# Kernel optimization log

Hardware: AMD Instinct MI355X
Metric: run time of the kernel (lower is better)

The kernel has to match this reference:

```python
import jax, jax.numpy as jnp
import numpy as np

B, N, PLANE, H, W = 2, 6, 64, 48, 48
HIDP = 64
PS = 3
RATES = 3


def conv2d(x, w, b, pad, dil=1):
    # x: [BN, Cin, H, W], w: [Cout, Cin, kh, kw]
    out = jax.lax.conv_general_dilated(
        x, w, window_strides=(1, 1),
        padding=[(pad, pad), (pad, pad)],
        rhs_dilation=(dil, dil),
        dimension_numbers=('NCHW', 'OIHW', 'NCHW'))
    return out + b[None, :, None, None]


def avgpool3(x):
    bn, c, h, w = x.shape
    return x.reshape(bn, c, h // PS, PS, w // PS, PS).mean(axis=(3, 5))


def setup_inputs() -> dict:
    key = jax.random.key(0)
    ks = jax.random.split(key, 20)
    s = 0.05
    hid_pa = PLANE * 3  # 192, hidden width of MultiFieldConv2d
    d = {
        'x': jax.random.normal(ks[0], (B, N, PLANE, H, W), jnp.float32),
        # patch_aggr: 3 dilated convs (rates 1..3), k=3, plane -> plane*3
        'pa_w1': jax.random.normal(ks[1], (hid_pa, PLANE, 3, 3)) * s,
        'pa_b1': jnp.zeros((hid_pa,)),
        'pa_w2': jax.random.normal(ks[2], (hid_pa, PLANE, 3, 3)) * s,
        'pa_b2': jnp.zeros((hid_pa,)),
        'pa_w3': jax.random.normal(ks[3], (hid_pa, PLANE, 3, 3)) * s,
        'pa_b3': jnp.zeros((hid_pa,)),
        # convert: 1x1 (hid_pa*rates -> 3*hidp), relu, 1x1 (3*hidp -> 3*hidp)
        'pa_cw1': jax.random.normal(ks[4], (3 * HIDP, hid_pa * RATES, 1, 1)) * s,
        'pa_cb1': jnp.zeros((3 * HIDP,)),
        'pa_cw2': jax.random.normal(ks[5], (3 * HIDP, 3 * HIDP, 1, 1)) * s,
        'pa_cb2': jnp.zeros((3 * HIDP,)),
        # to_kv conv: k=3 pad=1, hidp -> hidp
        'kv_w': jax.random.normal(ks[6], (HIDP, HIDP, 3, 3)) * s,
        'kv_b': jnp.zeros((HIDP,)),
        # to_out: 1x1 hidp->plane, relu, 1x1 plane->plane, relu
        'out_w1': jax.random.normal(ks[7], (PLANE, HIDP, 1, 1)) * s,
        'out_b1': jnp.zeros((PLANE,)),
        'out_w2': jax.random.normal(ks[8], (PLANE, PLANE, 1, 1)) * s,
        'out_b2': jnp.zeros((PLANE,)),
        'scales': jnp.ones((N,)),
    }
    return d


def reference(x, pa_w1, pa_b1, pa_w2, pa_b2, pa_w3, pa_b3,
              pa_cw1, pa_cb1, pa_cw2, pa_cb2,
              kv_w, kv_b, out_w1, out_b1, out_w2, out_b2, scales):
    b, n, c, h, w = x.shape
    scale = HIDP ** (-0.5)
    xf = x.reshape(b * n, c, h, w)

    # MultiFieldConv2d: dilated convs (same spatial size for odd k), concat, 1x1 convert
    u = jnp.concatenate([
        conv2d(xf, pa_w1, pa_b1, pad=1, dil=1),
        conv2d(xf, pa_w2, pa_b2, pad=2, dil=2),
        conv2d(xf, pa_w3, pa_b3, pad=3, dil=3),
    ], axis=1)
    qkv = conv2d(jax.nn.relu(conv2d(u, pa_cw1, pa_cb1, 0)), pa_cw2, pa_cb2, 0)
    qkv = jax.nn.relu(qkv)  # F.relu(patch_aggr(x))
    xq, xk, xv = jnp.split(qkv, 3, axis=1)  # each [BN, hidp, H, W]

    def to_kv(t):
        return avgpool3(jax.nn.relu(conv2d(t, kv_w, kv_b, pad=PS // 2)))

    k_ = to_kv(xk)                       # [BN, hidp, H/3, W/3]
    v_ = to_kv(xv) * (1.0 / PS ** 2)

    hw_kv = k_.shape[2] * k_.shape[3]
    Qs = xq.reshape(b, n, HIDP, h * w).transpose(0, 1, 3, 2)   # b n g d
    Ks = k_.reshape(b, n, HIDP, hw_kv).transpose(0, 1, 3, 2)   # b m k d
    Vs = v_.reshape(b, n, HIDP, hw_kv).transpose(0, 1, 3, 2)

    # Leave-one-out sigmoid attention: sum_{j != i} sigmoid(q_i k_j^T * scale) @ v_j
    # Computed as full sum minus the self (j == i) term (exact same math).
    A_all = jax.nn.sigmoid(jnp.einsum('bngd,bmkd->bngmk', Qs, Ks) * scale)
    out_all = jnp.einsum('bngmk,bmkd->bngd', A_all, Vs)
    A_self = jax.nn.sigmoid(jnp.einsum('bngd,bnkd->bngk', Qs, Ks) * scale)
    out_self = jnp.einsum('bngk,bnkd->bngd', A_self, Vs)
    attn_out = out_all - out_self                               # [b, n, HW, hidp]

    res = attn_out.transpose(0, 1, 3, 2).reshape(b, n, HIDP, h, w)
    xv5 = xv.reshape(b, n, HIDP, h, w)
    res = jax.nn.relu(res + scales[None, :, None, None, None] * xv5)

    rf = res.reshape(b * n, HIDP, h, w)
    o = jax.nn.relu(conv2d(jax.nn.relu(conv2d(rf, out_w1, out_b1, 0)), out_w2, out_b2, 0))
    return o.reshape(b, n, c, h, w)
```

## Files before the change

kernel.cpp:

```cpp
#include <hip/hip_runtime.h>
#include <hip/hip_bf16.h>
#include <math.h>

#define BB 2
#define NVIEW 6
#define BN 12
#define CIN 64
#define HH 48
#define WW 48
#define PP (HH*WW)
#define OC 192
#define HPA 192
#define HIDP 64
#define KHW 16
#define PK 256
#define PADW 54
#define PADA (PADW*PADW)
#define NTOT (BN*PP)
#define K1 1728
#define KVPW 50
#define KVPA (KVPW*KVPW)

typedef __attribute__((ext_vector_type(8))) short bf16x8;
typedef __attribute__((ext_vector_type(4))) float f32x4;

#define OFF_WEFFB 0
#define SZ_WEFFB_FL (OC*K1/2)
#define OFF_BEFF (OFF_WEFFB + SZ_WEFFB_FL)
#define SZ_BEFF 256
#define OFF_CW2B (OFF_BEFF + SZ_BEFF)
#define SZ_CW2B_FL (OC*OC/2)
#define OFF_WKVB (OFF_CW2B + SZ_CW2B_FL)
#define SZ_WKVB_FL (64*576/2)
#define OFF_PADXT (OFF_WKVB + SZ_WKVB_FL)
#define SZ_PADXT_FL (BN*PADA*64/2)
#define OFF_QB16 (OFF_PADXT + SZ_PADXT_FL)
#define SZ_QB16_FL (BN*PP*64/2)
#define OFF_KB16 (OFF_QB16 + SZ_QB16_FL)
#define SZ_KB16_FL (BN*PK*64/2)
#define OFF_VB16T (OFF_KB16 + SZ_KB16_FL)
#define SZ_VB16T_FL (BN*64*PK/2)
#define OFF_KVPAD (OFF_VB16T + SZ_VB16T_FL)
#define SZ_KVPAD_FL (BN*2*KVPA*64/2)
#define OFF_CONVB (OFF_KVPAD + SZ_KVPAD_FL)
#define SZ_CONVB_FL (BN*2*PP*64/2)
#define OFF_W1SW (OFF_CONVB + SZ_CONVB_FL)
#define SZ_WSW_FL 2048
#define OFF_W2SW (OFF_W1SW + SZ_WSW_FL)
#define OFF_ATTNP (OFF_W2SW + SZ_WSW_FL)
#define SZ_ATTNP (BN*PP*HIDP)
#define OFF_XVB16 (OFF_ATTNP + 2*SZ_ATTNP)
#define SZ_XVB16_FL (BN*PP*64/2)

__device__ __forceinline__ void load_lds16(const void* g, void* l) {
    __builtin_amdgcn_global_load_lds(
        (const __attribute__((address_space(1))) unsigned int*)g,
        (__attribute__((address_space(3))) unsigned int*)l, 16, 0, 0);
}

__device__ __forceinline__ unsigned short f2bu(float f) {
    __hip_bfloat16 h = __float2bfloat16(f);
    return *(unsigned short*)&h;
}

__device__ __forceinline__ float bu2f(unsigned short h) {
    unsigned int u = ((unsigned int)h) << 16;
    return *(float*)&u;
}

__global__ void k_fold(const float* __restrict__ cw1, const float* __restrict__ cb1,
                       const float* __restrict__ w1, const float* __restrict__ b1,
                       const float* __restrict__ w2, const float* __restrict__ b2,
                       const float* __restrict__ w3, const float* __restrict__ b3,
                       __hip_bfloat16* __restrict__ weffb, float* __restrict__ beff) {
    int r = blockIdx.x / OC;
    int o = blockIdx.x % OC;
    int t = threadIdx.x;
    int ic = t / 9, tap = t % 9;
    const float* w = (r==0) ? w1 : (r==1) ? w2 : w3;
    float acc = 0.f;
    for (int c = 0; c < HPA; ++c)
        acc += cw1[o*(HPA*3) + r*HPA + c] * w[c*(CIN*9) + t];
    weffb[(size_t)o*K1 + r*576 + tap*64 + ic] = __float2bfloat16(acc);
    if (r == 0 && t == 0) {
        float bacc = cb1[o];
        for (int rr = 0; rr < 3; ++rr) {
            const float* bb = (rr==0)?b1:(rr==1)?b2:b3;
            for (int c = 0; c < HPA; ++c)
                bacc += cw1[o*(HPA*3) + rr*HPA + c] * bb[c];
        }
        beff[o] = bacc;
    }
}

__global__ void k_wkvb(const float* __restrict__ kvw, __hip_bfloat16* __restrict__ wkvb) {
    int idx = blockIdx.x*256 + threadIdx.x;
    if (idx >= 64*576) return;
    int oc = idx / 576, rest = idx % 576;
    int tap = rest / 64, ic = rest % 64;
    wkvb[idx] = __float2bfloat16(kvw[(oc*64 + ic)*9 + tap]);
}

__global__ void k_wcvt(const float* __restrict__ cw2, __hip_bfloat16* __restrict__ cw2b) {
    int idx = blockIdx.x*256 + threadIdx.x;
    if (idx < OC*OC) cw2b[idx] = __float2bfloat16(cw2[idx]);
}

__global__ void k_wout(const float* __restrict__ w1, const float* __restrict__ w2,
                       __hip_bfloat16* __restrict__ w1sw, __hip_bfloat16* __restrict__ w2sw) {
    int idx = blockIdx.x*256 + threadIdx.x;
    if (idx >= 2*4096) return;
    const float* w = (idx < 4096) ? w1 : w2;
    __hip_bfloat16* dst = (idx < 4096) ? w1sw : w2sw;
    int i = idx & 4095;
    int oc = i >> 6, s = (i >> 3) & 7, e = i & 7;
    int k = ((s ^ (oc & 7)) << 3) + e;
    dst[i] = __float2bfloat16(w[oc*64 + k]);
}

__global__ void k_padxT(const float* __restrict__ x, __hip_bfloat16* __restrict__ padxT) {
    int idx = blockIdx.x*256 + threadIdx.x;
    if (idx >= BN*PADA) return;
    int spos = idx % PADA; int bn = idx / PADA;
    int sy = spos / PADW, sx = spos % PADW;
    __hip_bfloat16* dst = padxT + (size_t)idx*64;
    if (sy >= 3 && sy < 51 && sx >= 3 && sx < 51) {
        const float* src = x + (size_t)bn*CIN*PP + (sy-3)*WW + (sx-3);
        #pragma unroll 8
        for (int ic = 0; ic < 64; ++ic) dst[ic] = __float2bfloat16(src[ic*PP]);
    } else {
        #pragma unroll 8
        for (int ic = 0; ic < 64; ++ic) dst[ic] = __float2bfloat16(0.f);
    }
}

__global__ void k_zero(__hip_bfloat16* __restrict__ kvpad) {
    size_t idx = ((size_t)blockIdx.x*256 + threadIdx.x)*8;
    bf16x8 z = (bf16x8){0,0,0,0,0,0,0,0};
    *(bf16x8*)(kvpad + idx) = z;
}

__global__ __launch_bounds__(256) void k_gemm1(const __hip_bfloat16* __restrict__ wA,
        const __hip_bfloat16* __restrict__ pxT, const float* __restrict__ beff,
        __hip_bfloat16* __restrict__ hidbt) {
    __shared__ __align__(16) char smem[24576];
    int tid = threadIdx.x;
    int wid = tid >> 6, lane = tid & 63;
    int tileN = blockIdx.x * 128, tileM = blockIdx.y * 64;
    int sgr = ((lane&7) ^ (lane>>3)) * 8;

    size_t gbase[6];
    #pragma unroll
    for (int s2 = 0; s2 < 6; ++s2) {
        int seg = wid*6 + s2;
        if (seg < 8) {
            int row = seg*8 + (lane>>3);
            gbase[s2] = (size_t)(tileM + row)*K1 + sgr;
        } else {
            int n = tileN + (seg-8)*8 + (lane>>3);
            int bn = n / PP, p = n % PP;
            int py = p / WW, px = p % WW;
            gbase[s2] = ((size_t)bn*PADA + (py+3)*PADW + (px+3))*64 + sgr;
        }
    }
    int wr = wid >> 1, wc = wid & 1;
    int l7 = lane & 7, lh = lane >> 4;
    int arowb[2], browb[4];
    #pragma unroll
    for (int m = 0; m < 2; ++m)
        arowb[m] = (wr*32 + m*16 + (lane&15))*128;
    #pragma unroll
    for (int nf = 0; nf < 4; ++nf)
        browb[nf] = 8192 + (wc*64 + nf*16 + (lane&15))*128;

    f32x4 acc[2][4];
    #pragma unroll
    for (int m = 0; m < 2; ++m)
        #pragma unroll
        for (int nf = 0; nf < 4; ++nf) acc[m][nf] = (f32x4){0.f,0.f,0.f,0.f};

    for (int kt = 0; kt < 27; ++kt) {
        int r_ = kt / 9, tap = kt - r_*9;
        int dy = tap/3 - 1, dx = tap%3 - 1;
        int doff = (r_+1)*(dy*PADW + dx);
        __syncthreads();
        #pragma unroll
        for (int s2 = 0; s2 < 6; ++s2) {
            int seg = wid*6 + s2;
            const __hip_bfloat16* g = (seg < 8) ? wA + gbase[s2] + kt*64
                                                : pxT + gbase[s2] + (size_t)doff*64;
            load_lds16(g, smem + seg*1024);
        }
        __syncthreads();
        bf16x8 a[2][2], b[4][2];
        #pragma unroll
        for (int kk = 0; kk < 2; ++kk) {
            int gof = ((kk*4 + lh) ^ l7) << 4;
            #pragma unroll
            for (int m = 0; m < 2; ++m)
                a[m][kk] = *(const bf16x8*)(smem + arowb[m] + gof);
            #pragma unroll
            for (int nf = 0; nf < 4; ++nf)
                b[nf][kk] = *(const bf16x8*)(smem + browb[nf] + gof);
        }
        #pragma unroll
        for (int kk = 0; kk < 2; ++kk)
            #pragma unroll
            for (int m = 0; m < 2; ++m)
                #pragma unroll
                for (int nf = 0; nf < 4; ++nf)
                    acc[m][nf] = __builtin_amdgcn_mfma_f32_16x16x32_bf16(
                        a[m][kk], b[nf][kk], acc[m][nf], 0, 0, 0);
    }
    #pragma unroll
    for (int m = 0; m < 2; ++m) {
        int rbase = tileM + wr*32 + m*16 + (lane>>4)*4;
        float4 bz = *(const float4*)&beff[rbase];
        #pragma unroll
        for (int nf = 0; nf < 4; ++nf) {
            int col = tileN + wc*64 + nf*16 + (lane&15);
            union { ushort4 u; __hip_bfloat16 h[4]; } cv;
            cv.h[0] = __float2bfloat16(fmaxf(acc[m][nf][0] + bz.x, 0.f));
            cv.h[1] = __float2bfloat16(fmaxf(acc[m][nf][1] + bz.y, 0.f));
            cv.h[2] = __float2bfloat16(fmaxf(acc[m][nf][2] + bz.z, 0.f));
            cv.h[3] = __float2bfloat16(fmaxf(acc[m][nf][3] + bz.w, 0.f));
            *(ushort4*)&hidbt[(size_t)col*OC + rbase] = cv.u;
        }
    }
}

__global__ __launch_bounds__(256) void k_gemm2(const __hip_bfloat16* __restrict__ wA,
        const __hip_bfloat16* __restrict__ Bt, const float* __restrict__ cb2,
        __hip_bfloat16* __restrict__ xvb16, __hip_bfloat16* __restrict__ qb16,
        __hip_bfloat16* __restrict__ kvpad) {
    __shared__ __align__(16) char smem[24576];
    int tid = threadIdx.x;
    int wid = tid >> 6, lane = tid & 63;
    int tileN = blockIdx.x * 128, tileM = blockIdx.y * 64;
    int sgr = ((lane&7) ^ (lane>>3)) * 8;
    size_t gbase[6]; const __hip_bfloat16* gsrc[6];
    #pragma unroll
    for (int s2 = 0; s2 < 6; ++s2) {
        int seg = wid*6 + s2;
        if (seg < 8) {
            int row = seg*8 + (lane>>3);
            gbase[s2] = (size_t)(tileM + row)*OC + sgr;
            gsrc[s2] = wA;
        } else {
            int n = tileN + (seg-8)*8 + (lane>>3);
            gbase[s2] = (size_t)n*OC + sgr;
            gsrc[s2] = Bt;
        }
    }
    int wr = wid >> 1, wc = wid & 1;
    int l7 = lane & 7, lh = lane >> 4;
    int arowb[2], browb[4];
    #pragma unroll
    for (int m = 0; m < 2; ++m)
        arowb[m] = (wr*32 + m*16 + (lane&15))*128;
    #pragma unroll
    for (int nf = 0; nf < 4; ++nf)
        browb[nf] = 8192 + (wc*64 + nf*16 + (lane&15))*128;
    f32x4 acc[2][4];
    #pragma unroll
    for (int m = 0; m < 2; ++m)
        #pragma unroll
        for (int nf = 0; nf < 4; ++nf) acc[m][nf] = (f32x4){0.f,0.f,0.f,0.f};

    for (int kt = 0; kt < 3; ++kt) {
        __syncthreads();
        #pragma unroll
        for (int s2 = 0; s2 < 6; ++s2)
            load_lds16(gsrc[s2] + gbase[s2] + kt*64, smem + (wid*6+s2)*1024);
        __syncthreads();
        bf16x8 a[2][2], b[4][2];
        #pragma unroll
        for (int kk = 0; kk < 2; ++kk) {
            int gof = ((kk*4 + lh) ^ l7) << 4;
            #pragma unroll
            for (int m = 0; m < 2; ++m)
                a[m][kk] = *(const bf16x8*)(smem + arowb[m] + gof);
            #pragma unroll
            for (int nf = 0; nf < 4; ++nf)
                b[nf][kk] = *(const bf16x8*)(smem + browb[nf] + gof);
        }
        #pragma unroll
        for (int kk = 0; kk < 2; ++kk)
            #pragma unroll
            for (int m = 0; m < 2; ++m)
                #pragma unroll
                for (int nf = 0; nf < 4; ++nf)
                    acc[m][nf] = __builtin_amdgcn_mfma_f32_16x16x32_bf16(
                        a[m][kk], b[nf][kk], acc[m][nf], 0, 0, 0);
    }
    #pragma unroll
    for (int m = 0; m < 2; ++m) {
        int rbase = tileM + wr*32 + m*16 + (lane>>4)*4;
        float4 cz = *(const float4*)&cb2[rbase];
        #pragma unroll
        for (int nf = 0; nf < 4; ++nf) {
            int col = tileN + wc*64 + nf*16 + (lane&15);
            int bn = col / PP, p = col % PP;
            float v0 = fmaxf(acc[m][nf][0] + cz.x, 0.f);
            float v1 = fmaxf(acc[m][nf][1] + cz.y, 0.f);
            float v2 = fmaxf(acc[m][nf][2] + cz.z, 0.f);
            float v3 = fmaxf(acc[m][nf][3] + cz.w, 0.f);
            ushort4 bv;
            bv.x = f2bu(v0); bv.y = f2bu(v1); bv.z = f2bu(v2); bv.w = f2bu(v3);
            if (tileM == 0) {
                *(ushort4*)&qb16[(size_t)col*64 + rbase] = bv;
            } else {
                int kv = (tileM == 128) ? 1 : 0;
                int py = p / WW, px = p % WW;
                int d = rbase - tileM;
                *(ushort4*)&kvpad[((size_t)(bn*2+kv)*KVPA + (py+1)*KVPW + px+1)*64 + d] = bv;
                if (kv == 1)
                    *(ushort4*)&xvb16[(size_t)col*64 + d] = bv;
            }
        }
    }
}

__global__ __launch_bounds__(256) void k_kvgemm(const __hip_bfloat16* __restrict__ wA,
        const __hip_bfloat16* __restrict__ kvpad, const float* __restrict__ kvb,
        __hip_bfloat16* __restrict__ convb) {
    __shared__ __align__(16) char smem[24576];
    int tid = threadIdx.x;
    int wid = tid >> 6, lane = tid & 63;
    int tileN = blockIdx.x * 128;
    int bn2 = tileN / PP, p0 = tileN % PP;
    int sgr = ((lane&7) ^ (lane>>3)) * 8;

    size_t gbase[6];
    #pragma unroll
    for (int s2 = 0; s2 < 6; ++s2) {
        int seg = wid*6 + s2;
        if (seg < 8) {
            int row = seg*8 + (lane>>3);
            gbase[s2] = (size_t)row*576 + sgr;
        } else {
            int p = p0 + (seg-8)*8 + (lane>>3);
            int py = p / WW, px = p % WW;
            gbase[s2] = ((size_t)bn2*KVPA + (py+1)*KVPW + px+1)*64 + sgr;
        }
    }
    int wr = wid >> 1, wc = wid & 1;
    int l7 = lane & 7, lh = lane >> 4;
    int arowb[2], browb[4];
    #pragma unroll
    for (int m = 0; m < 2; ++m)
        arowb[m] = (wr*32 + m*16 + (lane&15))*128;
    #pragma unroll
    for (int nf = 0; nf < 4; ++nf)
        browb[nf] = 8192 + (wc*64 + nf*16 + (lane&15))*128;

    f32x4 acc[2][4];
    #pragma unroll
    for (int m = 0; m < 2; ++m)
        #pragma unroll
        for (int nf = 0; nf < 4; ++nf) acc[m][nf] = (f32x4){0.f,0.f,0.f,0.f};

    for (int kt = 0; kt < 9; ++kt) {
        int dy = kt/3 - 1, dx = kt%3 - 1;
        int doff = dy*KVPW + dx;
        __syncthreads();
        #pragma unroll
        for (int s2 = 0; s2 < 6; ++s2) {
            int seg = wid*6 + s2;
            const __hip_bfloat16* g = (seg < 8) ? wA + gbase[s2] + kt*64
                                                : kvpad + gbase[s2] + (size_t)doff*64;
            load_lds16(g, smem + seg*1024);
        }
        __syncthreads();
        bf16x8 a[2][2], b[4][2];
        #pragma unroll
        for (int kk = 0; kk < 2; ++kk) {
            int gof = ((kk*4 + lh) ^ l7) << 4;
            #pragma unroll
            for (int m = 0; m < 2; ++m)
                a[m][kk] = *(const bf16x8*)(smem + arowb[m] + gof);
            #pragma unroll
            for (int nf = 0; nf < 4; ++nf)
                b[nf][kk] = *(const bf16x8*)(smem + browb[nf] + gof);
        }
        #pragma unroll
        for (int kk = 0; kk < 2; ++kk)
            #pragma unroll
            for (int m = 0; m < 2; ++m)
                #pragma unroll
                for (int nf = 0; nf < 4; ++nf)
                    acc[m][nf] = __builtin_amdgcn_mfma_f32_16x16x32_bf16(
                        a[m][kk], b[nf][kk], acc[m][nf], 0, 0, 0);
    }
    #pragma unroll
    for (int m = 0; m < 2; ++m) {
        int rbase = wr*32 + m*16 + (lane>>4)*4;
        float4 bz = *(const float4*)&kvb[rbase];
        #pragma unroll
        for (int nf = 0; nf < 4; ++nf) {
            int col = p0 + wc*64 + nf*16 + (lane&15);
            ushort4 cv;
            cv.x = f2bu(fmaxf(acc[m][nf][0] + bz.x, 0.f));
            cv.y = f2bu(fmaxf(acc[m][nf][1] + bz.y, 0.f));
            cv.z = f2bu(fmaxf(acc[m][nf][2] + bz.z, 0.f));
            cv.w = f2bu(fmaxf(acc[m][nf][3] + bz.w, 0.f));
            *(ushort4*)&convb[((size_t)bn2*PP + col)*64 + rbase] = cv;
        }
    }
}

__global__ __launch_bounds__(256) void k_pool(const __hip_bfloat16* __restrict__ convb,
        __hip_bfloat16* __restrict__ kbufb, __hip_bfloat16* __restrict__ vbufT) {
    int idx = blockIdx.x*256 + threadIdx.x;
    int dg = idx % 8; idx /= 8;
    int pp = idx % PK; idx /= PK;
    int bn2 = idx;
    int kv = bn2 & 1, bn = bn2 >> 1;
    int qy = pp / KHW, qx = pp % KHW;
    float s[8] = {0,0,0,0,0,0,0,0};
    const __hip_bfloat16* base = convb + (size_t)bn2*PP*64 + dg*8;
    #pragma unroll
    for (int sy = 0; sy < 3; ++sy)
        #pragma unroll
        for (int sx = 0; sx < 3; ++sx) {
            union { bf16x8 v; unsigned short h[8]; } c;
            c.v = *(const bf16x8*)(base + ((size_t)(qy*3+sy)*WW + qx*3+sx)*64);
            #pragma unroll
            for (int j = 0; j < 8; ++j) s[j] += bu2f(c.h[j]);
        }
    if (kv == 0) {
        union { ushort4 u[2]; unsigned short h[8]; } cv;
        #pragma unroll
        for (int j = 0; j < 8; ++j) cv.h[j] = f2bu(s[j] * (1.f/9.f));
        ushort4* dst = (ushort4*)(kbufb + ((size_t)bn*PK + pp)*64 + dg*8);
        dst[0] = cv.u[0]; dst[1] = cv.u[1];
    } else {
        #pragma unroll
        for (int j = 0; j < 8; ++j)
            vbufT[((size_t)bn*64 + dg*8 + j)*PK + pp] = __float2bfloat16(s[j]*(1.f/81.f));
    }
}

__global__ __launch_bounds__(256) void k_attn3(const __hip_bfloat16* __restrict__ qb16,
        const __hip_bfloat16* __restrict__ kbufb, const __hip_bfloat16* __restrict__ vbufT,
        float* __restrict__ attnp) {
    __shared__ __align__(16) char smem[32768];
    char* Qs = smem;
    char* Ks = smem + 8192;
    char* Vs = smem + 16384;
    char* Ps = smem + 24576;
    int tid = threadIdx.x;
    int wid = tid >> 6, lane = tid & 63;
    int bid = blockIdx.x;
    int ks = bid & 1; bid >>= 1;
    int qt = bid % 36; int bn = bid / 36;
    int b = bn / NVIEW, n = bn % NVIEW;
    int p0 = qt*64;

    {
        const char* gq = (const char*)(qb16 + ((size_t)bn*PP + p0)*64);
        #pragma unroll
        for (int i = 0; i < 2; ++i) {
            int s = wid*2 + i;
            int lin = s*1024 + lane*16;
            int r = lin >> 7, c = (lin >> 4) & 7;
            int gof = (r<<7) + ((c ^ (r&7)) << 4);
            load_lds16(gq + gof, Qs + s*1024);
        }
    }
    int arow = wid*16 + (lane&15);
    int brow = lane&15;
    int gcol = lane>>4;
    int vrow = tid >> 2;
    int vc2 = (tid & 3) * 2;

    f32x4 oacc[4];
    #pragma unroll
    for (int i = 0; i < 4; ++i) oacc[i] = (f32x4){0,0,0,0};

    for (int mi = 0; mi < NVIEW-1; ++mi) {
        int m = mi + (mi >= n ? 1 : 0);
        int bnk = b*NVIEW + m;
        const char* gk = (const char*)(kbufb + (size_t)bnk*PK*64);
        const __hip_bfloat16* gv = vbufT + (size_t)bnk*64*PK;
        for (int kc = ks*2; kc < ks*2+2; ++kc) {
            __syncthreads();
            #pragma unroll
            for (int i = 0; i < 2; ++i) {
                int s = wid*2 + i;
                int lin = s*1024 + lane*16;
                int r = lin >> 7, c = (lin >> 4) & 7;
                int gof = (r<<7) + ((c ^ (r&7)) << 4);
                load_lds16(gk + (size_t)kc*8192 + gof, Ks + s*1024);
            }
            {
                const __hip_bfloat16* src = gv + vrow*PK + kc*64 + vc2*8;
                bf16x8 v0 = *(const bf16x8*)src;
                bf16x8 v1 = *(const bf16x8*)(src+8);
                *(bf16x8*)(Vs + vrow*128 + ((vc2 ^ (vrow&7))<<4)) = v0;
                *(bf16x8*)(Vs + vrow*128 + (((vc2+1) ^ (vrow&7))<<4)) = v1;
            }
            __syncthreads();
            f32x4 sacc[4];
            #pragma unroll
            for (int i = 0; i < 4; ++i) sacc[i] = (f32x4){0,0,0,0};
            #pragma unroll
            for (int kk = 0; kk < 2; ++kk) {
                int g = kk*4 + gcol;
                bf16x8 af = *(const bf16x8*)(Ks + arow*128 + ((g ^ (arow&7))<<4));
                #pragma unroll
                for (int nf = 0; nf < 4; ++nf) {
                    int q = nf*16 + brow;
                    bf16x8 bq = *(const bf16x8*)(Qs + q*128 + ((g ^ (q&7))<<4));
                    sacc[nf] = __builtin_amdgcn_mfma_f32_16x16x32_bf16(af, bq, sacc[nf], 0,0,0);
                }
            }
            {
                int kbase = wid*16 + gcol*4;
                #pragma unroll
                for (int nf = 0; nf < 4; ++nf) {
                    int q = nf*16 + brow;
                    ushort4 pu;
                    float e0 = __expf(-sacc[nf][0]*0.125f);
                    float e1 = __expf(-sacc[nf][1]*0.125f);
                    float e2 = __expf(-sacc[nf][2]*0.125f);
                    float e3 = __expf(-sacc[nf][3]*0.125f);
                    pu.x = f2bu(__builtin_amdgcn_rcpf(1.f+e0));
                    pu.y = f2bu(__builtin_amdgcn_rcpf(1.f+e1));
                    pu.z = f2bu(__builtin_amdgcn_rcpf(1.f+e2));
                    pu.w = f2bu(__builtin_amdgcn_rcpf(1.f+e3));
                    *(ushort4*)(Ps + q*128 + (((kbase>>3) ^ (q&7))<<4) + (kbase&7)*2) = pu;
                }
            }
            __syncthreads();
            #pragma unroll
            for (int kk = 0; kk < 2; ++kk) {
                int g = kk*4 + gcol;
                int qr = wid*16 + brow;
                bf16x8 pf = *(const bf16x8*)(Ps + qr*128 + ((g ^ (qr&7))<<4));
                #pragma unroll
                for (int nf = 0; nf < 4; ++nf) {
                    int d = nf*16 + brow;
                    bf16x8 vf = *(const bf16x8*)(Vs + d*128 + ((g ^ (d&7))<<4));
                    oacc[nf] = __builtin_amdgcn_mfma_f32_16x16x32_bf16(pf, vf, oacc[nf], 0,0,0);
                }
            }
        }
    }
    float* ab = attnp + (size_t)ks*SZ_ATTNP + ((size_t)bn*PP + p0)*64;
    #pragma unroll
    for (int nf = 0; nf < 4; ++nf) {
        #pragma unroll
        for (int r = 0; r < 4; ++r) {
            int q = wid*16 + gcol*4 + r;
            int d = nf*16 + brow;
            ab[(size_t)q*64 + d] = oacc[nf][r];
        }
    }
}

__global__ __launch_bounds__(256) void k_out2(const float* __restrict__ attnp,
        const __hip_bfloat16* __restrict__ xvb16, const float* __restrict__ scales,
        const __hip_bfloat16* __restrict__ w1sw, const __hip_bfloat16* __restrict__ w2sw,
        const float* __restrict__ b1, const float* __restrict__ b2,
        float* __restrict__ out) {
    __shared__ __align__(16) char smem[49152];
    char* W1s = smem;
    char* W2s = smem + 8192;
    char* Rs  = smem + 16384;
    char* Ts  = smem + 32768;
    int tid = threadIdx.x;
    int wid = tid >> 6, lane = tid & 63;
    int pix0 = blockIdx.x * 128;
    int bn = pix0 / PP;
    int pb = pix0 - bn*PP;
    float sc = scales[bn % NVIEW];

    #pragma unroll
    for (int i = 0; i < 4; ++i) {
        int seg = wid*4 + i;
        const char* src = (seg < 8) ? (const char*)w1sw + seg*1024
                                    : (const char*)w2sw + (seg-8)*1024;
        load_lds16(src + lane*16, smem + seg*1024);
    }
    {
        int p = tid >> 1, d0 = (tid & 1) * 32;
        int P = pix0 + p;
        const float* a0 = attnp + (size_t)P*64 + d0;
        const float* a1 = a0 + SZ_ATTNP;
        const __hip_bfloat16* xv = xvb16 + (size_t)P*64 + d0;
        #pragma unroll
        for (int j = 0; j < 4; ++j) {
            float4 u0 = *(const float4*)(a0 + j*8);
            float4 u1 = *(const float4*)(a0 + j*8 + 4);
            float4 v0 = *(const float4*)(a1 + j*8);
            float4 v1 = *(const float4*)(a1 + j*8 + 4);
            union { bf16x8 v; unsigned short h[8]; } xu;
            xu.v = *(const bf16x8*)(xv + j*8);
            union { bf16x8 v; unsigned short h[8]; } rv;
            rv.h[0] = f2bu(fmaxf(u0.x + v0.x + sc*bu2f(xu.h[0]), 0.f));
            rv.h[1] = f2bu(fmaxf(u0.y + v0.y + sc*bu2f(xu.h[1]), 0.f));
            rv.h[2] = f2bu(fmaxf(u0.z + v0.z + sc*bu2f(xu.h[2]), 0.f));
            rv.h[3] = f2bu(fmaxf(u0.w + v0.w + sc*bu2f(xu.h[3]), 0.f));
            rv.h[4] = f2bu(fmaxf(u1.x + v1.x + sc*bu2f(xu.h[4]), 0.f));
            rv.h[5] = f2bu(fmaxf(u1.y + v1.y + sc*bu2f(xu.h[5]), 0.f));
            rv.h[6] = f2bu(fmaxf(u1.z + v1.z + sc*bu2f(xu.h[6]), 0.f));
            rv.h[7] = f2bu(fmaxf(u1.w + v1.w + sc*bu2f(xu.h[7]), 0.f));
            int g = (d0 >> 3) + j;
            *(bf16x8*)(Rs + p*128 + ((g ^ (p&7)) << 4)) = rv.v;
        }
    }
    __syncthreads();

    int wr = wid >> 1, wc = wid & 1;
    int rrow = lane & 15, gcol = lane >> 4;
    f32x4 acc1[2][4];
    #pragma unroll
    for (int m = 0; m < 2; ++m)
        #pragma unroll
        for (int nf = 0; nf < 4; ++nf) acc1[m][nf] = (f32x4){0,0,0,0};
    #pragma unroll
    for (int kk = 0; kk < 2; ++kk) {
        int g = kk*4 + gcol;
        #pragma unroll
        for (int m = 0; m < 2; ++m) {
            int oc = wr*32 + m*16 + rrow;
            bf16x8 af = *(const bf16x8*)(W1s + oc*128 + ((g ^ (oc&7)) << 4));
            #pragma unroll
            for (int nf = 0; nf < 4; ++nf) {
                int px = wc*64 + nf*16 + rrow;
                bf16x8 bf = *(const bf16x8*)(Rs + px*128 + ((g ^ (px&7)) << 4));
                acc1[m][nf] = __builtin_amdgcn_mfma_f32_16x16x32_bf16(af, bf, acc1[m][nf], 0,0,0);
            }
        }
    }
    #pragma unroll
    for (int m = 0; m < 2; ++m) {
        int oc0 = wr*32 + m*16 + gcol*4;
        float4 bz = *(const float4*)&b1[oc0];
        #pragma unroll
        for (int nf = 0; nf < 4; ++nf) {
            int px = wc*64 + nf*16 + rrow;
            ushort4 tv;
            tv.x = f2bu(fmaxf(acc1[m][nf][0] + bz.x, 0.f));
            tv.y = f2bu(fmaxf(acc1[m][nf][1] + bz.y, 0.f));
            tv.z = f2bu(fmaxf(acc1[m][nf][2] + bz.z, 0.f));
            tv.w = f2bu(fmaxf(acc1[m][nf][3] + bz.w, 0.f));
            *(ushort4*)(Ts + px*128 + (((oc0>>3) ^ (px&7)) << 4) + (oc0&7)*2) = tv;
        }
    }
    __syncthreads();
    f32x4 acc2[2][4];
    #pragma unroll
    for (int m = 0; m < 2; ++m)
        #pragma unroll
        for (int nf = 0; nf < 4; ++nf) acc2[m][nf] = (f32x4){0,0,0,0};
    #pragma unroll
    for (int kk = 0; kk < 2; ++kk) {
        int g = kk*4 + gcol;
        #pragma unroll
        for (int m = 0; m < 2; ++m) {
            int oc = wr*32 + m*16 + rrow;
            bf16x8 af = *(const bf16x8*)(W2s + oc*128 + ((g ^ (oc&7)) << 4));
            #pragma unroll
            for (int nf = 0; nf < 4; ++nf) {
                int px = wc*64 + nf*16 + rrow;
                bf16x8 bf = *(const bf16x8*)(Ts + px*128 + ((g ^ (px&7)) << 4));
                acc2[m][nf] = __builtin_amdgcn_mfma_f32_16x16x32_bf16(af, bf, acc2[m][nf], 0,0,0);
            }
        }
    }
    #pragma unroll
    for (int m = 0; m < 2; ++m) {
        int oc0 = wr*32 + m*16 + gcol*4;
        float4 bz = *(const float4*)&b2[oc0];
        #pragma unroll
        for (int nf = 0; nf < 4; ++nf) {
            int px = wc*64 + nf*16 + rrow;
            float* dst = out + ((size_t)bn*64 + oc0)*PP + pb + px;
            dst[0*PP] = fmaxf(acc2[m][nf][0] + bz.x, 0.f);
            dst[1*PP] = fmaxf(acc2[m][nf][1] + bz.y, 0.f);
            dst[2*PP] = fmaxf(acc2[m][nf][2] + bz.z, 0.f);
            dst[3*PP] = fmaxf(acc2[m][nf][3] + bz.w, 0.f);
        }
    }
}

extern "C" void kernel_launch(void* const* d_in, const int* in_sizes, int n_in,
                              void* d_out, int out_size, void* d_ws, size_t ws_size,
                              hipStream_t stream) {
    (void)in_sizes; (void)n_in; (void)out_size; (void)ws_size;
    const float* x      = (const float*)d_in[0];
    const float* pa_w1  = (const float*)d_in[1];
    const float* pa_b1  = (const float*)d_in[2];
    const float* pa_w2  = (const float*)d_in[3];
    const float* pa_b2  = (const float*)d_in[4];
    const float* pa_w3  = (const float*)d_in[5];
    const float* pa_b3  = (const float*)d_in[6];
    const float* pa_cw1 = (const float*)d_in[7];
    const float* pa_cb1 = (const float*)d_in[8];
    const float* pa_cw2 = (const float*)d_in[9];
    const float* pa_cb2 = (const float*)d_in[10];
    const float* kv_w   = (const float*)d_in[11];
    const float* kv_b   = (const float*)d_in[12];
    const float* out_w1 = (const float*)d_in[13];
    const float* out_b1 = (const float*)d_in[14];
    const float* out_w2 = (const float*)d_in[15];
    const float* out_b2 = (const float*)d_in[16];
    const float* scales = (const float*)d_in[17];
    float* out = (float*)d_out;
    float* ws  = (float*)d_ws;

    __hip_bfloat16* weffb = (__hip_bfloat16*)(ws + OFF_WEFFB);
    float* beff = ws + OFF_BEFF;
    __hip_bfloat16* cw2b  = (__hip_bfloat16*)(ws + OFF_CW2B);
    __hip_bfloat16* wkvb  = (__hip_bfloat16*)(ws + OFF_WKVB);
    __hip_bfloat16* padxT = (__hip_bfloat16*)(ws + OFF_PADXT);
    __hip_bfloat16* qb16  = (__hip_bfloat16*)(ws + OFF_QB16);
    __hip_bfloat16* kbufb = (__hip_bfloat16*)(ws + OFF_KB16);
    __hip_bfloat16* vbufT = (__hip_bfloat16*)(ws + OFF_VB16T);
    __hip_bfloat16* kvpad = (__hip_bfloat16*)(ws + OFF_KVPAD);
    __hip_bfloat16* convb = (__hip_bfloat16*)(ws + OFF_CONVB);
    __hip_bfloat16* w1sw  = (__hip_bfloat16*)(ws + OFF_W1SW);
    __hip_bfloat16* w2sw  = (__hip_bfloat16*)(ws + OFF_W2SW);
    __hip_bfloat16* hidbt = (__hip_bfloat16*)(ws + OFF_ATTNP);
    float* attnp = ws + OFF_ATTNP;
    __hip_bfloat16* xvb16 = (__hip_bfloat16*)(ws + OFF_XVB16);

    k_fold<<<3*OC, CIN*9, 0, stream>>>(pa_cw1, pa_cb1, pa_w1, pa_b1,
                                       pa_w2, pa_b2, pa_w3, pa_b3, weffb, beff);
    k_wkvb<<<(64*576+255)/256, 256, 0, stream>>>(kv_w, wkvb);
    k_wcvt<<<(OC*OC+255)/256, 256, 0, stream>>>(pa_cw2, cw2b);
    k_wout<<<(2*4096+255)/256, 256, 0, stream>>>(out_w1, out_w2, w1sw, w2sw);
    k_padxT<<<(BN*PADA+255)/256, 256, 0, stream>>>(x, padxT);
    k_zero<<<(BN*2*KVPA*64/8)/256, 256, 0, stream>>>(kvpad);
    k_gemm1<<<dim3(NTOT/128, 3), 256, 0, stream>>>(weffb, padxT, beff, hidbt);
    k_gemm2<<<dim3(NTOT/128, 3), 256, 0, stream>>>(cw2b, hidbt, pa_cb2, xvb16, qb16, kvpad);
    k_kvgemm<<<BN*2*PP/128, 256, 0, stream>>>(wkvb, kvpad, kv_b, convb);
    k_pool<<<BN*2*PK*8/256, 256, 0, stream>>>(convb, kbufb, vbufT);
    k_attn3<<<BN*36*2, 256, 0, stream>>>(qb16, kbufb, vbufT, attnp);
    k_out2<<<NTOT/128, 256, 0, stream>>>(attnp, xvb16, scales, w1sw, w2sw,
                                         out_b1, out_b2, out);
}
```

Baseline: 122.2 us.

## Fuse dilated-conv GEMM and 1x1 convert GEMM into one kernel via LDS

Result: no change. 122.8 us (+0.5%).

```diff
diff --git a/kernel.cpp b/kernel.cpp
--- a/kernel.cpp
+++ b/kernel.cpp
@@ -93,29 +93,27 @@
     }
 }
 
-__global__ void k_wkvb(const float* __restrict__ kvw, __hip_bfloat16* __restrict__ wkvb) {
+__global__ void k_wprep(const float* __restrict__ kvw, const float* __restrict__ cw2,
+                        const float* __restrict__ w1, const float* __restrict__ w2,
+                        __hip_bfloat16* __restrict__ wkvb, __hip_bfloat16* __restrict__ cw2b,
+                        __hip_bfloat16* __restrict__ w1sw, __hip_bfloat16* __restrict__ w2sw) {
     int idx = blockIdx.x*256 + threadIdx.x;
-    if (idx >= 64*576) return;
-    int oc = idx / 576, rest = idx % 576;
-    int tap = rest / 64, ic = rest % 64;
-    wkvb[idx] = __float2bfloat16(kvw[(oc*64 + ic)*9 + tap]);
-}
-
-__global__ void k_wcvt(const float* __restrict__ cw2, __hip_bfloat16* __restrict__ cw2b) {
-    int idx = blockIdx.x*256 + threadIdx.x;
-    if (idx < OC*OC) cw2b[idx] = __float2bfloat16(cw2[idx]);
-}
-
-__global__ void k_wout(const float* __restrict__ w1, const float* __restrict__ w2,
-                       __hip_bfloat16* __restrict__ w1sw, __hip_bfloat16* __restrict__ w2sw) {
-    int idx = blockIdx.x*256 + threadIdx.x;
-    if (idx >= 2*4096) return;
-    const float* w = (idx < 4096) ? w1 : w2;
-    __hip_bfloat16* dst = (idx < 4096) ? w1sw : w2sw;
-    int i = idx & 4095;
-    int oc = i >> 6, s = (i >> 3) & 7, e = i & 7;
-    int k = ((s ^ (oc & 7)) << 3) + e;
-    dst[i] = __float2bfloat16(w[oc*64 + k]);
+    if (idx < 36864) {
+        int oc = idx / 576, rest = idx % 576;
+        int tap = rest / 64, ic = rest % 64;
+        wkvb[idx] = __float2bfloat16(kvw[(oc*64 + ic)*9 + tap]);
+    } else if (idx < 73728) {
+        int i = idx - 36864;
+        cw2b[i] = __float2bfloat16(cw2[i]);
+    } else if (idx < 81920) {
+        int i = idx - 73728;
+        const float* w = (i < 4096) ? w1 : w2;
+        __hip_bfloat16* dst = (i < 4096) ? w1sw : w2sw;
+        int j = i & 4095;
+        int oc = j >> 6, s = (j >> 3) & 7, e = j & 7;
+        int k = ((s ^ (oc & 7)) << 3) + e;
+        dst[j] = __float2bfloat16(w[oc*64 + k]);
+    }
 }
 
 __global__ void k_padxT(const float* __restrict__ x, __hip_bfloat16* __restrict__ padxT) {
@@ -140,182 +138,151 @@
     *(bf16x8*)(kvpad + idx) = z;
 }
 
-__global__ __launch_bounds__(256) void k_gemm1(const __hip_bfloat16* __restrict__ wA,
-        const __hip_bfloat16* __restrict__ pxT, const float* __restrict__ beff,
-        __hip_bfloat16* __restrict__ hidbt) {
-    __shared__ __align__(16) char smem[24576];
+__global__ __launch_bounds__(512) void k_mfc(const __hip_bfloat16* __restrict__ wA,
+        const __hip_bfloat16* __restrict__ pxT, const __hip_bfloat16* __restrict__ cw2b,
+        const float* __restrict__ beff, const float* __restrict__ cb2,
+        __hip_bfloat16* __restrict__ xvb16, __hip_bfloat16* __restrict__ qb16,
+        __hip_bfloat16* __restrict__ kvpad) {
+    __shared__ __align__(16) char smem[58368];
     int tid = threadIdx.x;
     int wid = tid >> 6, lane = tid & 63;
-    int tileN = blockIdx.x * 128, tileM = blockIdx.y * 64;
+    int bn = blockIdx.x / 18;
+    int pb = (blockIdx.x % 18) * 128;
     int sgr = ((lane&7) ^ (lane>>3)) * 8;
-
-    size_t gbase[6];
-    #pragma unroll
-    for (int s2 = 0; s2 < 6; ++s2) {
-        int seg = wid*6 + s2;
-        if (seg < 8) {
+    int wr = wid >> 1, wc = wid & 1;
+    int l7 = lane & 7, lh = lane >> 4, rrow = lane & 15, gcol = lane >> 4;
+
+    size_t gbase[5];
+    #pragma unroll
+    for (int s2 = 0; s2 < 5; ++s2) {
+        int seg = wid*5 + s2;
+        if (seg < 24) {
             int row = seg*8 + (lane>>3);
-            gbase[s2] = (size_t)(tileM + row)*K1 + sgr;
+            gbase[s2] = (size_t)row*K1 + sgr;
         } else {
-            int n = tileN + (seg-8)*8 + (lane>>3);
-            int bn = n / PP, p = n % PP;
+            int p = pb + (seg-24)*8 + (lane>>3);
             int py = p / WW, px = p % WW;
             gbase[s2] = ((size_t)bn*PADA + (py+3)*PADW + (px+3))*64 + sgr;
         }
     }
-    int wr = wid >> 1, wc = wid & 1;
-    int l7 = lane & 7, lh = lane >> 4;
-    int arowb[2], browb[4];
-    #pragma unroll
-    for (int m = 0; m < 2; ++m)
-        arowb[m] = (wr*32 + m*16 + (lane&15))*128;
-    #pragma unroll
-    for (int nf = 0; nf < 4; ++nf)
-        browb[nf] = 8192 + (wc*64 + nf*16 + (lane&15))*128;
-
-    f32x4 acc[2][4];
-    #pragma unroll
-    for (int m = 0; m < 2; ++m)
-        #pragma unroll
-        for (int nf = 0; nf < 4; ++nf) acc[m][nf] = (f32x4){0.f,0.f,0.f,0.f};
+
+    f32x4 acc1[3][4];
+    #pragma unroll
+    for (int m = 0; m < 3; ++m)
+        #pragma unroll
+        for (int nf = 0; nf < 4; ++nf) acc1[m][nf] = (f32x4){0.f,0.f,0.f,0.f};
 
     for (int kt = 0; kt < 27; ++kt) {
         int r_ = kt / 9, tap = kt - r_*9;
-        int dy = tap/3 - 1, dx = tap%3 - 1;
-        int doff = (r_+1)*(dy*PADW + dx);
+        int doff = (r_+1)*((tap/3 - 1)*PADW + (tap%3 - 1));
         __syncthreads();
         #pragma unroll
-        for (int s2 = 0; s2 < 6; ++s2) {
-            int seg = wid*6 + s2;
-            const __hip_bfloat16* g = (seg < 8) ? wA + gbase[s2] + kt*64
-                                                : pxT + gbase[s2] + (size_t)doff*64;
+        for (int s2 = 0; s2 < 5; ++s2) {
+            int seg = wid*5 + s2;
+            const __hip_bfloat16* g = (seg < 24) ? wA + gbase[s2] + kt*64
+                                                 : pxT + gbase[s2] + (size_t)doff*64;
             load_lds16(g, smem + seg*1024);
         }
         __syncthreads();
-        bf16x8 a[2][2], b[4][2];
+        bf16x8 a[3][2], b[4][2];
         #pragma unroll
         for (int kk = 0; kk < 2; ++kk) {
             int gof = ((kk*4 + lh) ^ l7) << 4;
             #pragma unroll
-            for (int m = 0; m < 2; ++m)
-                a[m][kk] = *(const bf16x8*)(smem + arowb[m] + gof);
+            for (int m = 0; m < 3; ++m)
+                a[m][kk] = *(const bf16x8*)(smem + (wr*48 + m*16 + rrow)*128 + gof);
             #pragma unroll
             for (int nf = 0; nf < 4; ++nf)
-                b[nf][kk] = *(const bf16x8*)(smem + browb[nf] + gof);
+                b[nf][kk] = *(const bf16x8*)(smem + 24576 + (wc*64 + nf*16 + rrow)*128 + gof);
         }
         #pragma unroll
         for (int kk = 0; kk < 2; ++kk)
             #pragma unroll
-            for (int m = 0; m < 2; ++m)
+            for (int m = 0; m < 3; ++m)
                 #pragma unroll
                 for (int nf = 0; nf < 4; ++nf)
-                    acc[m][nf] = __builtin_amdgcn_mfma_f32_16x16x32_bf16(
-                        a[m][kk], b[nf][kk], acc[m][nf], 0, 0, 0);
-    }
-    #pragma unroll
-    for (int m = 0; m < 2; ++m) {
-        int rbase = tileM + wr*32 + m*16 + (lane>>4)*4;
-        float4 bz = *(const float4*)&beff[rbase];
-        #pragma unroll
-        for (int nf = 0; nf < 4; ++nf) {
-            int col = tileN + wc*64 + nf*16 + (lane&15);
-            union { ushort4 u; __hip_bfloat16 h[4]; } cv;
-            cv.h[0] = __float2bfloat16(fmaxf(acc[m][nf][0] + bz.x, 0.f));
-            cv.h[1] = __float2bfloat16(fmaxf(acc[m][nf][1] + bz.y, 0.f));
-            cv.h[2] = __float2bfloat16(fmaxf(acc[m][nf][2] + bz.z, 0.f));
-            cv.h[3] = __float2bfloat16(fmaxf(acc[m][nf][3] + bz.w, 0.f));
-            *(ushort4*)&hidbt[(size_t)col*OC + rbase] = cv.u;
-        }
-    }
-}
-
-__global__ __launch_bounds__(256) void k_gemm2(const __hip_bfloat16* __restrict__ wA,
-        const __hip_bfloat16* __restrict__ Bt, const float* __restrict__ cb2,
-        __hip_bfloat16* __restrict__ xvb16, __hip_bfloat16* __restrict__ qb16,
-        __hip_bfloat16* __restrict__ kvpad) {
-    __shared__ __align__(16) char smem[24576];
-    int tid = threadIdx.x;
-    int wid = tid >> 6, lane = tid & 63;
-    int tileN = blockIdx.x * 128, tileM = blockIdx.y * 64;
-    int sgr = ((lane&7) ^ (lane>>3)) * 8;
-    size_t gbase[6]; const __hip_bfloat16* gsrc[6];
-    #pragma unroll
-    for (int s2 = 0; s2 < 6; ++s2) {
-        int seg = wid*6 + s2;
-        if (seg < 8) {
+                    acc1[m][nf] = __builtin_amdgcn_mfma_f32_16x16x32_bf16(
+                        a[m][kk], b[nf][kk], acc1[m][nf], 0, 0, 0);
+    }
+
+    f32x4 acc2[3][4];
+    #pragma unroll
+    for (int m = 0; m < 3; ++m)
+        #pragma unroll
+        for (int nf = 0; nf < 4; ++nf) acc2[m][nf] = (f32x4){0.f,0.f,0.f,0.f};
+
+    for (int kt2 = 0; kt2 < 3; ++kt2) {
+        __syncthreads();
+        #pragma unroll
+        for (int s2 = 0; s2 < 3; ++s2) {
+            int seg = wid*3 + s2;
             int row = seg*8 + (lane>>3);
-            gbase[s2] = (size_t)(tileM + row)*OC + sgr;
-            gsrc[s2] = wA;
-        } else {
-            int n = tileN + (seg-8)*8 + (lane>>3);
-            gbase[s2] = (size_t)n*OC + sgr;
-            gsrc[s2] = Bt;
-        }
-    }
-    int wr = wid >> 1, wc = wid & 1;
-    int l7 = lane & 7, lh = lane >> 4;
-    int arowb[2], browb[4];
-    #pragma unroll
-    for (int m = 0; m < 2; ++m)
-        arowb[m] = (wr*32 + m*16 + (lane&15))*128;
-    #pragma unroll
-    for (int nf = 0; nf < 4; ++nf)
-        browb[nf] = 8192 + (wc*64 + nf*16 + (lane&15))*128;
-    f32x4 acc[2][4];
-    #pragma unroll
-    for (int m = 0; m < 2; ++m)
-        #pragma unroll
-        for (int nf = 0; nf < 4; ++nf) acc[m][nf] = (f32x4){0.f,0.f,0.f,0.f};
-
-    for (int kt = 0; kt < 3; ++kt) {
+            load_lds16(cw2b + (size_t)row*OC + kt2*64 + sgr, smem + seg*1024);
+        }
+        #pragma unroll
+        for (int m = 0; m < 3; ++m) {
+            int oc16 = wr*48 + m*16;
+            if ((oc16 >> 6) == kt2) {
+                int oc0 = oc16 + gcol*4;
+                float4 bz = *(const float4*)&beff[oc0];
+                int cb = (oc0 - kt2*64)*2;
+                #pragma unroll
+                for (int nf = 0; nf < 4; ++nf) {
+                    int px = wc*64 + nf*16 + rrow;
+                    ushort4 hv;
+                    hv.x = f2bu(fmaxf(acc1[m][nf][0] + bz.x, 0.f));
+                    hv.y = f2bu(fmaxf(acc1[m][nf][1] + bz.y, 0.f));
+                    hv.z = f2bu(fmaxf(acc1[m][nf][2] + bz.z, 0.f));
+                    hv.w = f2bu(fmaxf(acc1[m][nf][3] + bz.w, 0.f));
+                    *(ushort4*)(smem + 40960 + px*136 + cb) = hv;
+                }
+            }
+        }
         __syncthreads();
         #pragma unroll
-        for (int s2 = 0; s2 < 6; ++s2)
-            load_lds16(gsrc[s2] + gbase[s2] + kt*64, smem + (wid*6+s2)*1024);
-        __syncthreads();
-        bf16x8 a[2][2], b[4][2];
-        #pragma unroll
         for (int kk = 0; kk < 2; ++kk) {
-            int gof = ((kk*4 + lh) ^ l7) << 4;
-            #pragma unroll
-            for (int m = 0; m < 2; ++m)
-                a[m][kk] = *(const bf16x8*)(smem + arowb[m] + gof);
+            int gofA = ((kk*4 + lh) ^ l7) << 4;
+            int gofB = (kk*4 + lh) << 4;
+            bf16x8 a2[3], b2[4];
+            #pragma unroll
+            for (int m2 = 0; m2 < 3; ++m2)
+                a2[m2] = *(const bf16x8*)(smem + (wr*48 + m2*16 + rrow)*128 + gofA);
             #pragma unroll
             for (int nf = 0; nf < 4; ++nf)
-                b[nf][kk] = *(const bf16x8*)(smem + browb[nf] + gof);
-        }
-        #pragma unroll
-        for (int kk = 0; kk < 2; ++kk)
-            #pragma unroll
-            for (int m = 0; m < 2; ++m)
+                b2[nf] = *(const bf16x8*)(smem + 40960 + (wc*64 + nf*16 + rrow)*136 + gofB);
+            #pragma unroll
+            for (int m2 = 0; m2 < 3; ++m2)
                 #pragma unroll
                 for (int nf = 0; nf < 4; ++nf)
-                    acc[m][nf] = __builtin_amdgcn_mfma_f32_16x16x32_bf16(
-                        a[m][kk], b[nf][kk], acc[m][nf], 0, 0, 0);
-    }
-    #pragma unroll
-    for (int m = 0; m < 2; ++m) {
-        int rbase = tileM + wr*32 + m*16 + (lane>>4)*4;
-        float4 cz = *(const float4*)&cb2[rbase];
+                    acc2[m2][nf] = __builtin_amdgcn_mfma_f32_16x16x32_bf16(
+                        a2[m2], b2[nf], acc2[m2][nf], 0, 0, 0);
+        }
+    }
+
+    #pragma unroll
+    for (int m2 = 0; m2 < 3; ++m2) {
+        int oc16 = wr*48 + m2*16;
+        int sec = oc16 >> 6;
+        int oc0 = oc16 + gcol*4;
+        float4 cz = *(const float4*)&cb2[oc0];
         #pragma unroll
         for (int nf = 0; nf < 4; ++nf) {
-            int col = tileN + wc*64 + nf*16 + (lane&15);
-            int bn = col / PP, p = col % PP;
-            float v0 = fmaxf(acc[m][nf][0] + cz.x, 0.f);
-            float v1 = fmaxf(acc[m][nf][1] + cz.y, 0.f);
-            float v2 = fmaxf(acc[m][nf][2] + cz.z, 0.f);
-            float v3 = fmaxf(acc[m][nf][3] + cz.w, 0.f);
+            int px = wc*64 + nf*16 + rrow;
+            int p = pb + px;
             ushort4 bv;
-            bv.x = f2bu(v0); bv.y = f2bu(v1); bv.z = f2bu(v2); bv.w = f2bu(v3);
-            if (tileM == 0) {
-                *(ushort4*)&qb16[(size_t)col*64 + rbase] = bv;
+            bv.x = f2bu(fmaxf(acc2[m2][nf][0] + cz.x, 0.f));
+            bv.y = f2bu(fmaxf(acc2[m2][nf][1] + cz.y, 0.f));
+            bv.z = f2bu(fmaxf(acc2[m2][nf][2] + cz.z, 0.f));
+            bv.w = f2bu(fmaxf(acc2[m2][nf][3] + cz.w, 0.f));
+            if (sec == 0) {
+                *(ushort4*)&qb16[((size_t)bn*PP + p)*64 + oc0] = bv;
             } else {
-                int kv = (tileM == 128) ? 1 : 0;
-                int py = p / WW, px = p % WW;
-                int d = rbase - tileM;
-                *(ushort4*)&kvpad[((size_t)(bn*2+kv)*KVPA + (py+1)*KVPW + px+1)*64 + d] = bv;
+                int kv = sec - 1;
+                int py = p / WW, pxx = p % WW;
+                int d = oc0 - (sec << 6);
+                *(ushort4*)&kvpad[((size_t)(bn*2+kv)*KVPA + (py+1)*KVPW + pxx+1)*64 + d] = bv;
                 if (kv == 1)
-                    *(ushort4*)&xvb16[(size_t)col*64 + d] = bv;
+                    *(ushort4*)&xvb16[((size_t)bn*PP + p)*64 + d] = bv;
             }
         }
     }
@@ -723,19 +690,17 @@
     __hip_bfloat16* convb = (__hip_bfloat16*)(ws + OFF_CONVB);
     __hip_bfloat16* w1sw  = (__hip_bfloat16*)(ws + OFF_W1SW);
     __hip_bfloat16* w2sw  = (__hip_bfloat16*)(ws + OFF_W2SW);
-    __hip_bfloat16* hidbt = (__hip_bfloat16*)(ws + OFF_ATTNP);
     float* attnp = ws + OFF_ATTNP;
     __hip_bfloat16* xvb16 = (__hip_bfloat16*)(ws + OFF_XVB16);
 
     k_fold<<<3*OC, CIN*9, 0, stream>>>(pa_cw1, pa_cb1, pa_w1, pa_b1,
                                        pa_w2, pa_b2, pa_w3, pa_b3, weffb, beff);
-    k_wkvb<<<(64*576+255)/256, 256, 0, stream>>>(kv_w, wkvb);
-    k_wcvt<<<(OC*OC+255)/256, 256, 0, stream>>>(pa_cw2, cw2b);
-    k_wout<<<(2*4096+255)/256, 256, 0, stream>>>(out_w1, out_w2, w1sw, w2sw);
+    k_wprep<<<320, 256, 0, stream>>>(kv_w, pa_cw2, out_w1, out_w2,
+                                     wkvb, cw2b, w1sw, w2sw);
     k_padxT<<<(BN*PADA+255)/256, 256, 0, stream>>>(x, padxT);
     k_zero<<<(BN*2*KVPA*64/8)/256, 256, 0, stream>>>(kvpad);
-    k_gemm1<<<dim3(NTOT/128, 3), 256, 0, stream>>>(weffb, padxT, beff, hidbt);
-    k_gemm2<<<dim3(NTOT/128, 3), 256, 0, stream>>>(cw2b, hidbt, pa_cb2, xvb16, qb16, kvpad);
+    k_mfc<<<NTOT/128, 512, 0, stream>>>(weffb, padxT, cw2b, beff, pa_cb2,
+                                        xvb16, qb16, kvpad);
     k_kvgemm<<<BN*2*PP/128, 256, 0, stream>>>(wkvb, kvpad, kv_b, convb);
     k_pool<<<BN*2*PK*8/256, 256, 0, stream>>>(convb, kbufb, vbufT);
     k_attn3<<<BN*36*2, 256, 0, stream>>>(qb16, kbufb, vbufT, attnp);
```
